# Kernel tuning notes

Hardware: AMD Instinct MI355X
Metric: run time of the kernel (lower is better)

The kernel has to match this reference:

```python
import jax, jax.numpy as jnp
import numpy as np

N, C, H, W = 8, 256, 64, 64
Q_REDUCE, K_REDUCE, V_REDUCE = 8, 8, 1


def setup_inputs() -> dict:
    key = jax.random.key(0)
    ks = jax.random.split(key, 6)
    Cq, Ck, Cv = C // Q_REDUCE, C // K_REDUCE, C // V_REDUCE
    s = 0.02
    x = jax.random.normal(ks[0], (N, C, H, W), dtype=jnp.float32)
    Wq = jax.random.normal(ks[1], (Cq, C), dtype=jnp.float32) * s
    Wk = jax.random.normal(ks[2], (Ck, C), dtype=jnp.float32) * s
    Wv = jax.random.normal(ks[3], (Cv, C), dtype=jnp.float32) * s
    Wo = jax.random.normal(ks[4], (C, Cv), dtype=jnp.float32) * s
    gamma = jax.random.normal(ks[5], (), dtype=jnp.float32)  # trained scalar (init 0.0 in torch)
    return {"x": x, "Wq": Wq, "Wk": Wk, "Wv": Wv, "Wo": Wo, "gamma": gamma}


def reference(x, Wq, Wk, Wv, Wo, gamma):
    n, c, h, w = x.shape
    xf = x.reshape(n, c, h * w)                      # [N, C, HW]
    q = jnp.einsum('qc,ncl->nql', Wq, xf)            # [N, Cq, HW] (1x1 conv)
    k = jnp.einsum('kc,ncl->nkl', Wk, xf)            # [N, Ck, HW]
    v = jnp.einsum('vc,ncl->nvl', Wv, xf)            # [N, Cv, HW]
    e = jnp.einsum('nci,ncj->nij', q, k)             # [N, HW, HW], unscaled energies
    a = jax.nn.softmax(e, axis=-1)                   # softmax over keys j
    o = jnp.einsum('nvi,nij->nvj', v, a)             # [N, Cv, HW]  (o = bmm(v, a))
    o = o.reshape(n, -1, w, h)                       # faithful: view(N,-1,W,H)
    out = jnp.einsum('ov,nvhw->nohw', Wo, o)         # output 1x1 conv
    return gamma * out
```

## Files before the change

kernel.cpp:

```cpp
#include <hip/hip_runtime.h>
#include <hip/hip_bf16.h>

#define NB 8
#define CIN 256
#define LL 4096
#define CQ 32
#define CV 256

typedef __attribute__((ext_vector_type(8))) short bf16x8;
typedef __attribute__((ext_vector_type(4))) float f32x4;

__device__ __forceinline__ unsigned short f2bf(float f) {
    union { __hip_bfloat16 h; unsigned short u; } c;
    c.h = __float2bfloat16(f);
    return c.u;
}
__device__ __forceinline__ float bf2f(unsigned short h) {
    return __uint_as_float(((unsigned)h) << 16);
}

__global__ __launch_bounds__(256) void k_wcast(
    const float* __restrict__ Wq, const float* __restrict__ Wk,
    const float* __restrict__ Wv, const float* __restrict__ Wo,
    unsigned short* __restrict__ Wb, unsigned short* __restrict__ Wob)
{
    const float LOG2E = 1.4426950408889634f;
    const int row = blockIdx.x, t = threadIdx.x;
    if (row < 320) {
        float val;
        if (row < 32)      val = Wq[row * 256 + t] * LOG2E;
        else if (row < 64) val = Wk[(row - 32) * 256 + t];
        else               val = Wv[(row - 64) * 256 + t];
        Wb[row * 256 + t] = f2bf(val);
    } else {
        const int r2 = row - 320;
        Wob[r2 * 256 + t] = f2bf(Wo[r2 * 256 + t]);
    }
}

__global__ __launch_bounds__(512) void k_qkv3(
    const float* __restrict__ x, const unsigned short* __restrict__ Wb,
    unsigned short* __restrict__ qkt, unsigned short* __restrict__ v)
{
    __shared__ unsigned short xlds[64][264];
    __shared__ unsigned short tr[64][72];
    const int n = blockIdx.y, l0 = blockIdx.x * 64, t = threadIdx.x;
    const int w = t >> 6, lane = t & 63, lid = lane & 15, quad = lane >> 4;

    #pragma unroll
    for (int part = 0; part < 4; part++) {
        const int cbase = part * 64 + w * 8;
        float tmp[8];
        #pragma unroll
        for (int cc = 0; cc < 8; cc++)
            tmp[cc] = x[((size_t)n * CIN + cbase + cc) * LL + l0 + lane];
        bf16x8 s;
        #pragma unroll
        for (int cc = 0; cc < 8; cc++) s[cc] = (short)f2bf(tmp[cc]);
        *(bf16x8*)&xlds[lane][cbase] = s;
    }
    __syncthreads();

    const f32x4 fzero = {0.f, 0.f, 0.f, 0.f};
    f32x4 acc[3][4];
    #pragma unroll
    for (int mt = 0; mt < 3; mt++)
        #pragma unroll
        for (int nt = 0; nt < 4; nt++) acc[mt][nt] = fzero;

    for (int k0 = 0; k0 < 256; k0 += 32) {
        bf16x8 bx[4];
        #pragma unroll
        for (int nt = 0; nt < 4; nt++)
            bx[nt] = *(const bf16x8*)&xlds[nt * 16 + lid][k0 + quad * 8];
        #pragma unroll
        for (int vt = 0; vt < 2; vt++) {
            const bf16x8 wa = *(const bf16x8*)&Wb[(64 + w * 32 + vt * 16 + lid) * 256 + k0 + quad * 8];
            #pragma unroll
            for (int nt = 0; nt < 4; nt++)
                acc[vt][nt] = __builtin_amdgcn_mfma_f32_16x16x32_bf16(wa, bx[nt], acc[vt][nt], 0, 0, 0);
        }
        if (w < 4) {
            const bf16x8 wa = *(const bf16x8*)&Wb[(w * 16 + lid) * 256 + k0 + quad * 8];
            #pragma unroll
            for (int nt = 0; nt < 4; nt++)
                acc[2][nt] = __builtin_amdgcn_mfma_f32_16x16x32_bf16(wa, bx[nt], acc[2][nt], 0, 0, 0);
        }
    }
    #pragma unroll
    for (int vt = 0; vt < 2; vt++)
        #pragma unroll
        for (int nt = 0; nt < 4; nt++)
            #pragma unroll
            for (int reg = 0; reg < 4; reg++) {
                const int vr = w * 32 + vt * 16 + quad * 4 + reg;
                v[((size_t)n * CV + vr) * LL + l0 + nt * 16 + lid] = f2bf(acc[vt][nt][reg]);
            }
    if (w < 4) {
        #pragma unroll
        for (int nt = 0; nt < 4; nt++)
            #pragma unroll
            for (int reg = 0; reg < 4; reg++)
                tr[nt * 16 + lid][w * 16 + quad * 4 + reg] = f2bf(acc[2][nt][reg]);
    }
    __syncthreads();
    {
        const int l = t >> 3, c = (t & 7) * 8;
        *(uint4*)&qkt[((size_t)n * LL + l0 + l) * 64 + c] = *(const uint4*)&tr[l][c];
    }
}

__global__ __launch_bounds__(512) void k_rowsum3(
    const unsigned short* __restrict__ qkt, float* __restrict__ lns)
{
    __shared__ float red[64];
    const int n = blockIdx.y, i0 = blockIdx.x * 64, t = threadIdx.x;
    const int w = t >> 6, lid = t & 15, quad = (t & 63) >> 4;
    if (t < 64) red[t] = 0.f;
    __syncthreads();

    bf16x8 aq[4];
    #pragma unroll
    for (int mt = 0; mt < 4; mt++)
        aq[mt] = *(const bf16x8*)&qkt[((size_t)n * LL + i0 + mt * 16 + lid) * 64 + quad * 8];

    const f32x4 fzero = {0.f, 0.f, 0.f, 0.f};
    float sums[4][4];
    #pragma unroll
    for (int mt = 0; mt < 4; mt++)
        #pragma unroll
        for (int reg = 0; reg < 4; reg++) sums[mt][reg] = 0.f;

    for (int jt = 0; jt < 8; jt++) {
        const int j0 = jt * 512 + w * 64;
        bf16x8 bk[4];
        #pragma unroll
        for (int nt = 0; nt < 4; nt++)
            bk[nt] = *(const bf16x8*)&qkt[((size_t)n * LL + j0 + nt * 16 + lid) * 64 + 32 + quad * 8];
        #pragma unroll
        for (int mt = 0; mt < 4; mt++)
            #pragma unroll
            for (int nt = 0; nt < 4; nt++) {
                f32x4 e = __builtin_amdgcn_mfma_f32_16x16x32_bf16(aq[mt], bk[nt], fzero, 0, 0, 0);
                sums[mt][0] += __builtin_amdgcn_exp2f(e[0]);
                sums[mt][1] += __builtin_amdgcn_exp2f(e[1]);
                sums[mt][2] += __builtin_amdgcn_exp2f(e[2]);
                sums[mt][3] += __builtin_amdgcn_exp2f(e[3]);
            }
    }
    #pragma unroll
    for (int mt = 0; mt < 4; mt++)
        #pragma unroll
        for (int reg = 0; reg < 4; reg++) {
            float s = sums[mt][reg];
            s += __shfl_xor(s, 1); s += __shfl_xor(s, 2);
            s += __shfl_xor(s, 4); s += __shfl_xor(s, 8);
            if (lid == 0) atomicAdd(&red[mt * 16 + quad * 4 + reg], s);
        }
    __syncthreads();
    if (t < 64) lns[(size_t)n * LL + i0 + t] = -__builtin_log2f(red[t]);
}

__global__ __launch_bounds__(512, 4) void k_attn8(
    const unsigned short* __restrict__ qkt, const unsigned short* __restrict__ v,
    const float* __restrict__ lns, const unsigned short* __restrict__ Wob,
    const float* __restrict__ gp, float* __restrict__ out)
{
    __shared__ unsigned short pbuf[2][4][4][64][8];
    __shared__ unsigned short olds[64][264];

    const int bid = blockIdx.x;
    const int n = bid & 7, j0 = (bid >> 3) * 64, t = threadIdx.x;
    const int w = t >> 6, lane = t & 63, lid = lane & 15, quad = lane >> 4;
    const int kbw = w >> 1;
    const int qr = (w & 1) * 2 + (quad >> 1);
    const int e0 = (quad & 1) * 4;

    const unsigned short* qrow = qkt + ((size_t)n * LL + w * 16 + lid) * 64 + quad * 8;
    const float* lrow = lns + (size_t)n * LL + w * 16 + quad * 4;
    const unsigned short* vrow = v + ((size_t)n * CV + w * 32 + lid) * LL + quad * 8;

    bf16x8 bk[4];
    #pragma unroll
    for (int nt = 0; nt < 4; nt++)
        bk[nt] = *(const bf16x8*)&qkt[((size_t)n * LL + j0 + nt * 16 + lid) * 64 + 32 + quad * 8];

    const f32x4 fzero = {0.f, 0.f, 0.f, 0.f};
    f32x4 acc[2][4];
    #pragma unroll
    for (int mt = 0; mt < 2; mt++)
        #pragma unroll
        for (int nt = 0; nt < 4; nt++) acc[mt][nt] = fzero;

    bf16x8 aq = *(const bf16x8*)qrow;
    f32x4 lnsC = *(const f32x4*)lrow;
    {
        f32x4 e[4];
        #pragma unroll
        for (int nt = 0; nt < 4; nt++)
            e[nt] = __builtin_amdgcn_mfma_f32_16x16x32_bf16(aq, bk[nt], lnsC, 0, 0, 0);
        aq = *(const bf16x8*)(qrow + (size_t)128 * 64);
        lnsC = *(const f32x4*)(lrow + 128);
        #pragma unroll
        for (int nt = 0; nt < 4; nt++) {
            ushort4 s;
            s.x = f2bf(__builtin_amdgcn_exp2f(e[nt][0]));
            s.y = f2bf(__builtin_amdgcn_exp2f(e[nt][1]));
            s.z = f2bf(__builtin_amdgcn_exp2f(e[nt][2]));
            s.w = f2bf(__builtin_amdgcn_exp2f(e[nt][3]));
            *(ushort4*)&pbuf[0][nt][kbw][qr * 16 + lid][e0] = s;
        }
    }
    bf16x8 av[8];
    #pragma unroll
    for (int mt = 0; mt < 2; mt++)
        #pragma unroll
        for (int h = 0; h < 4; h++)
            av[mt * 4 + h] = *(const bf16x8*)(vrow + (size_t)mt * 16 * LL + h * 32);
    __syncthreads();

    for (int ic = 0; ic < 31; ic++) {
        const int cur = ic & 1;
        const size_t i0 = (size_t)ic * 128;
        f32x4 e2[4];
        #pragma unroll
        for (int nt = 0; nt < 4; nt++)
            e2[nt] = __builtin_amdgcn_mfma_f32_16x16x32_bf16(aq, bk[nt], lnsC, 0, 0, 0);
        const size_t ipf = (ic < 30) ? (i0 + 256) : i0;
        aq = *(const bf16x8*)(qrow + ipf * 64);
        lnsC = *(const f32x4*)(lrow + ipf);
        #pragma unroll
        for (int nt = 0; nt < 4; nt++) {
            ushort4 s;
            s.x = f2bf(__builtin_amdgcn_exp2f(e2[nt][0]));
            s.y = f2bf(__builtin_amdgcn_exp2f(e2[nt][1]));
            s.z = f2bf(__builtin_amdgcn_exp2f(e2[nt][2]));
            s.w = f2bf(__builtin_amdgcn_exp2f(e2[nt][3]));
            *(ushort4*)&pbuf[cur ^ 1][nt][kbw][qr * 16 + lid][e0] = s;
        }
        #pragma unroll
        for (int h = 0; h < 4; h++) {
            bf16x8 bp[4];
            #pragma unroll
            for (int nt = 0; nt < 4; nt++)
                bp[nt] = *(const bf16x8*)&pbuf[cur][nt][h][lane][0];
            #pragma unroll
            for (int mt = 0; mt < 2; mt++)
                #pragma unroll
                for (int nt = 0; nt < 4; nt++)
                    acc[mt][nt] = __builtin_amdgcn_mfma_f32_16x16x32_bf16(av[mt * 4 + h], bp[nt], acc[mt][nt], 0, 0, 0);
            #pragma unroll
            for (int mt = 0; mt < 2; mt++)
                av[mt * 4 + h] = *(const bf16x8*)(vrow + (size_t)mt * 16 * LL + (i0 + 128) + h * 32);
        }
        __syncthreads();
    }
    #pragma unroll
    for (int h = 0; h < 4; h++) {
        bf16x8 bp[4];
        #pragma unroll
        for (int nt = 0; nt < 4; nt++)
            bp[nt] = *(const bf16x8*)&pbuf[1][nt][h][lane][0];
        #pragma unroll
        for (int mt = 0; mt < 2; mt++)
            #pragma unroll
            for (int nt = 0; nt < 4; nt++)
                acc[mt][nt] = __builtin_amdgcn_mfma_f32_16x16x32_bf16(av[mt * 4 + h], bp[nt], acc[mt][nt], 0, 0, 0);
    }
    __syncthreads();

    #pragma unroll
    for (int mt = 0; mt < 2; mt++)
        #pragma unroll
        for (int nt = 0; nt < 4; nt++) {
            ushort4 s;
            s.x = f2bf(acc[mt][nt][0]); s.y = f2bf(acc[mt][nt][1]);
            s.z = f2bf(acc[mt][nt][2]); s.w = f2bf(acc[mt][nt][3]);
            *(ushort4*)&olds[nt * 16 + lid][w * 32 + mt * 16 + quad * 4] = s;
        }
    __syncthreads();
    f32x4 oacc[2][4];
    #pragma unroll
    for (int mt = 0; mt < 2; mt++)
        #pragma unroll
        for (int nt = 0; nt < 4; nt++) oacc[mt][nt] = fzero;
    for (int k0 = 0; k0 < 256; k0 += 32) {
        bf16x8 bo[4];
        #pragma unroll
        for (int nt = 0; nt < 4; nt++)
            bo[nt] = *(const bf16x8*)&olds[nt * 16 + lid][k0 + quad * 8];
        #pragma unroll
        for (int mt = 0; mt < 2; mt++) {
            const bf16x8 wa = *(const bf16x8*)&Wob[(w * 32 + mt * 16 + lid) * 256 + k0 + quad * 8];
            #pragma unroll
            for (int nt = 0; nt < 4; nt++)
                oacc[mt][nt] = __builtin_amdgcn_mfma_f32_16x16x32_bf16(wa, bo[nt], oacc[mt][nt], 0, 0, 0);
        }
    }
    const float g = *gp;
    #pragma unroll
    for (int mt = 0; mt < 2; mt++)
        #pragma unroll
        for (int nt = 0; nt < 4; nt++)
            #pragma unroll
            for (int reg = 0; reg < 4; reg++) {
                const int r = w * 32 + mt * 16 + quad * 4 + reg;
                out[((size_t)n * CIN + r) * LL + j0 + nt * 16 + lid] = g * oacc[mt][nt][reg];
            }
}

extern "C" void kernel_launch(void* const* d_in, const int* in_sizes, int n_in,
                              void* d_out, int out_size, void* d_ws, size_t ws_size,
                              hipStream_t stream) {
    const float* x     = (const float*)d_in[0];
    const float* Wq    = (const float*)d_in[1];
    const float* Wk    = (const float*)d_in[2];
    const float* Wv    = (const float*)d_in[3];
    const float* Wo    = (const float*)d_in[4];
    const float* gamma = (const float*)d_in[5];

    unsigned short* qkt = (unsigned short*)d_ws;
    unsigned short* v   = qkt + (size_t)NB * LL * 64;
    unsigned short* Wb  = v + (size_t)NB * CV * LL;
    unsigned short* Wob = Wb + 320 * 256;
    float* lns          = (float*)(Wob + 256 * 256);
    float* out = (float*)d_out;

    k_wcast  <<<dim3(576),   256, 0, stream>>>(Wq, Wk, Wv, Wo, Wb, Wob);
    k_qkv3   <<<dim3(64, 8), 512, 0, stream>>>(x, Wb, qkt, v);
    k_rowsum3<<<dim3(64, 8), 512, 0, stream>>>(qkt, lns);
    k_attn8  <<<dim3(512),   512, 0, stream>>>(qkt, v, lns, Wob, gamma, out);
}
```

Baseline: 263.4 us.

## Halve attention output tile to 32 columns, double grid, shrink V register prefetch

```diff
diff --git a/kernel.cpp b/kernel.cpp
--- a/kernel.cpp
+++ b/kernel.cpp
@@ -161,16 +161,16 @@
     if (t < 64) lns[(size_t)n * LL + i0 + t] = -__builtin_log2f(red[t]);
 }
 
-__global__ __launch_bounds__(512, 4) void k_attn8(
+__global__ __launch_bounds__(512, 6) void k_attn11(
     const unsigned short* __restrict__ qkt, const unsigned short* __restrict__ v,
     const float* __restrict__ lns, const unsigned short* __restrict__ Wob,
     const float* __restrict__ gp, float* __restrict__ out)
 {
-    __shared__ unsigned short pbuf[2][4][4][64][8];
-    __shared__ unsigned short olds[64][264];
+    __shared__ unsigned short pbuf[2][2][4][64][8];
+    __shared__ unsigned short olds[32][264];
 
     const int bid = blockIdx.x;
-    const int n = bid & 7, j0 = (bid >> 3) * 64, t = threadIdx.x;
+    const int n = bid & 7, j0 = (bid >> 3) * 32, t = threadIdx.x;
     const int w = t >> 6, lane = t & 63, lid = lane & 15, quad = lane >> 4;
     const int kbw = w >> 1;
     const int qr = (w & 1) * 2 + (quad >> 1);
@@ -180,29 +180,33 @@
     const float* lrow = lns + (size_t)n * LL + w * 16 + quad * 4;
     const unsigned short* vrow = v + ((size_t)n * CV + w * 32 + lid) * LL + quad * 8;
 
-    bf16x8 bk[4];
-    #pragma unroll
-    for (int nt = 0; nt < 4; nt++)
+    bf16x8 bk[2];
+    #pragma unroll
+    for (int nt = 0; nt < 2; nt++)
         bk[nt] = *(const bf16x8*)&qkt[((size_t)n * LL + j0 + nt * 16 + lid) * 64 + 32 + quad * 8];
 
     const f32x4 fzero = {0.f, 0.f, 0.f, 0.f};
-    f32x4 acc[2][4];
-    #pragma unroll
-    for (int mt = 0; mt < 2; mt++)
-        #pragma unroll
-        for (int nt = 0; nt < 4; nt++) acc[mt][nt] = fzero;
+    f32x4 acc[2][2];
+    #pragma unroll
+    for (int mt = 0; mt < 2; mt++)
+        #pragma unroll
+        for (int nt = 0; nt < 2; nt++) acc[mt][nt] = fzero;
 
     bf16x8 aq = *(const bf16x8*)qrow;
     f32x4 lnsC = *(const f32x4*)lrow;
+    bf16x8 avA[2], avB[2];
+    #pragma unroll
+    for (int mt = 0; mt < 2; mt++)
+        avA[mt] = *(const bf16x8*)(vrow + (size_t)mt * 16 * LL + 0);
     {
-        f32x4 e[4];
-        #pragma unroll
-        for (int nt = 0; nt < 4; nt++)
+        f32x4 e[2];
+        #pragma unroll
+        for (int nt = 0; nt < 2; nt++)
             e[nt] = __builtin_amdgcn_mfma_f32_16x16x32_bf16(aq, bk[nt], lnsC, 0, 0, 0);
         aq = *(const bf16x8*)(qrow + (size_t)128 * 64);
         lnsC = *(const f32x4*)(lrow + 128);
         #pragma unroll
-        for (int nt = 0; nt < 4; nt++) {
+        for (int nt = 0; nt < 2; nt++) {
             ushort4 s;
             s.x = f2bf(__builtin_amdgcn_exp2f(e[nt][0]));
             s.y = f2bf(__builtin_amdgcn_exp2f(e[nt][1]));
@@ -211,26 +215,20 @@
             *(ushort4*)&pbuf[0][nt][kbw][qr * 16 + lid][e0] = s;
         }
     }
-    bf16x8 av[8];
-    #pragma unroll
-    for (int mt = 0; mt < 2; mt++)
-        #pragma unroll
-        for (int h = 0; h < 4; h++)
-            av[mt * 4 + h] = *(const bf16x8*)(vrow + (size_t)mt * 16 * LL + h * 32);
     __syncthreads();
 
     for (int ic = 0; ic < 31; ic++) {
         const int cur = ic & 1;
         const size_t i0 = (size_t)ic * 128;
-        f32x4 e2[4];
-        #pragma unroll
-        for (int nt = 0; nt < 4; nt++)
+        f32x4 e2[2];
+        #pragma unroll
+        for (int nt = 0; nt < 2; nt++)
             e2[nt] = __builtin_amdgcn_mfma_f32_16x16x32_bf16(aq, bk[nt], lnsC, 0, 0, 0);
         const size_t ipf = (ic < 30) ? (i0 + 256) : i0;
         aq = *(const bf16x8*)(qrow + ipf * 64);
         lnsC = *(const f32x4*)(lrow + ipf);
         #pragma unroll
-        for (int nt = 0; nt < 4; nt++) {
+        for (int nt = 0; nt < 2; nt++) {
             ushort4 s;
             s.x = f2bf(__builtin_amdgcn_exp2f(e2[nt][0]));
             s.y = f2bf(__builtin_amdgcn_exp2f(e2[nt][1]));
@@ -238,62 +236,125 @@
             s.w = f2bf(__builtin_amdgcn_exp2f(e2[nt][3]));
             *(ushort4*)&pbuf[cur ^ 1][nt][kbw][qr * 16 + lid][e0] = s;
         }
-        #pragma unroll
-        for (int h = 0; h < 4; h++) {
-            bf16x8 bp[4];
-            #pragma unroll
-            for (int nt = 0; nt < 4; nt++)
-                bp[nt] = *(const bf16x8*)&pbuf[cur][nt][h][lane][0];
-            #pragma unroll
-            for (int mt = 0; mt < 2; mt++)
-                #pragma unroll
-                for (int nt = 0; nt < 4; nt++)
-                    acc[mt][nt] = __builtin_amdgcn_mfma_f32_16x16x32_bf16(av[mt * 4 + h], bp[nt], acc[mt][nt], 0, 0, 0);
-            #pragma unroll
-            for (int mt = 0; mt < 2; mt++)
-                av[mt * 4 + h] = *(const bf16x8*)(vrow + (size_t)mt * 16 * LL + (i0 + 128) + h * 32);
-        }
+        bf16x8 bp[2];
+        #pragma unroll
+        for (int mt = 0; mt < 2; mt++)
+            avB[mt] = *(const bf16x8*)(vrow + (size_t)mt * 16 * LL + i0 + 32);
+        #pragma unroll
+        for (int nt = 0; nt < 2; nt++)
+            bp[nt] = *(const bf16x8*)&pbuf[cur][nt][0][lane][0];
+        #pragma unroll
+        for (int mt = 0; mt < 2; mt++)
+            #pragma unroll
+            for (int nt = 0; nt < 2; nt++)
+                acc[mt][nt] = __builtin_amdgcn_mfma_f32_16x16x32_bf16(avA[mt], bp[nt], acc[mt][nt], 0, 0, 0);
+        #pragma unroll
+        for (int mt = 0; mt < 2; mt++)
+            avA[mt] = *(const bf16x8*)(vrow + (size_t)mt * 16 * LL + i0 + 64);
+        #pragma unroll
+        for (int nt = 0; nt < 2; nt++)
+            bp[nt] = *(const bf16x8*)&pbuf[cur][nt][1][lane][0];
+        #pragma unroll
+        for (int mt = 0; mt < 2; mt++)
+            #pragma unroll
+            for (int nt = 0; nt < 2; nt++)
+                acc[mt][nt] = __builtin_amdgcn_mfma_f32_16x16x32_bf16(avB[mt], bp[nt], acc[mt][nt], 0, 0, 0);
+        #pragma unroll
+        for (int mt = 0; mt < 2; mt++)
+            avB[mt] = *(const bf16x8*)(vrow + (size_t)mt * 16 * LL + i0 + 96);
+        #pragma unroll
+        for (int nt = 0; nt < 2; nt++)
+            bp[nt] = *(const bf16x8*)&pbuf[cur][nt][2][lane][0];
+        #pragma unroll
+        for (int mt = 0; mt < 2; mt++)
+            #pragma unroll
+            for (int nt = 0; nt < 2; nt++)
+                acc[mt][nt] = __builtin_amdgcn_mfma_f32_16x16x32_bf16(avA[mt], bp[nt], acc[mt][nt], 0, 0, 0);
+        #pragma unroll
+        for (int mt = 0; mt < 2; mt++)
+            avA[mt] = *(const bf16x8*)(vrow + (size_t)mt * 16 * LL + i0 + 128);
+        #pragma unroll
+        for (int nt = 0; nt < 2; nt++)
+            bp[nt] = *(const bf16x8*)&pbuf[cur][nt][3][lane][0];
+        #pragma unroll
+        for (int mt = 0; mt < 2; mt++)
+            #pragma unroll
+            for (int nt = 0; nt < 2; nt++)
+                acc[mt][nt] = __builtin_amdgcn_mfma_f32_16x16x32_bf16(avB[mt], bp[nt], acc[mt][nt], 0, 0, 0);
         __syncthreads();
     }
-    #pragma unroll
-    for (int h = 0; h < 4; h++) {
-        bf16x8 bp[4];
-        #pragma unroll
-        for (int nt = 0; nt < 4; nt++)
-            bp[nt] = *(const bf16x8*)&pbuf[1][nt][h][lane][0];
-        #pragma unroll
-        for (int mt = 0; mt < 2; mt++)
-            #pragma unroll
-            for (int nt = 0; nt < 4; nt++)
-                acc[mt][nt] = __builtin_amdgcn_mfma_f32_16x16x32_bf16(av[mt * 4 + h], bp[nt], acc[mt][nt], 0, 0, 0);
-    }
-    __syncthreads();
-
-    #pragma unroll
-    for (int mt = 0; mt < 2; mt++)
-        #pragma unroll
-        for (int nt = 0; nt < 4; nt++) {
+    {
+        const size_t i0 = (size_t)31 * 128;
+        bf16x8 bp[2];
+        #pragma unroll
+        for (int mt = 0; mt < 2; mt++)
+            avB[mt] = *(const bf16x8*)(vrow + (size_t)mt * 16 * LL + i0 + 32);
+        #pragma unroll
+        for (int nt = 0; nt < 2; nt++)
+            bp[nt] = *(const bf16x8*)&pbuf[1][nt][0][lane][0];
+        #pragma unroll
+        for (int mt = 0; mt < 2; mt++)
+            #pragma unroll
+            for (int nt = 0; nt < 2; nt++)
+                acc[mt][nt] = __builtin_amdgcn_mfma_f32_16x16x32_bf16(avA[mt], bp[nt], acc[mt][nt], 0, 0, 0);
+        #pragma unroll
+        for (int mt = 0; mt < 2; mt++)
+            avA[mt] = *(const bf16x8*)(vrow + (size_t)mt * 16 * LL + i0 + 64);
+        #pragma unroll
+        for (int nt = 0; nt < 2; nt++)
+            bp[nt] = *(const bf16x8*)&pbuf[1][nt][1][lane][0];
+        #pragma unroll
+        for (int mt = 0; mt < 2; mt++)
+            #pragma unroll
+            for (int nt = 0; nt < 2; nt++)
+                acc[mt][nt] = __builtin_amdgcn_mfma_f32_16x16x32_bf16(avB[mt], bp[nt], acc[mt][nt], 0, 0, 0);
+        #pragma unroll
+        for (int mt = 0; mt < 2; mt++)
+            avB[mt] = *(const bf16x8*)(vrow + (size_t)mt * 16 * LL + i0 + 96);
+        #pragma unroll
+        for (int nt = 0; nt < 2; nt++)
+            bp[nt] = *(const bf16x8*)&pbuf[1][nt][2][lane][0];
+        #pragma unroll
+        for (int mt = 0; mt < 2; mt++)
+            #pragma unroll
+            for (int nt = 0; nt < 2; nt++)
+                acc[mt][nt] = __builtin_amdgcn_mfma_f32_16x16x32_bf16(avA[mt], bp[nt], acc[mt][nt], 0, 0, 0);
+        #pragma unroll
+        for (int nt = 0; nt < 2; nt++)
+            bp[nt] = *(const bf16x8*)&pbuf[1][nt][3][lane][0];
+        #pragma unroll
+        for (int mt = 0; mt < 2; mt++)
+            #pragma unroll
+            for (int nt = 0; nt < 2; nt++)
+                acc[mt][nt] = __builtin_amdgcn_mfma_f32_16x16x32_bf16(avB[mt], bp[nt], acc[mt][nt], 0, 0, 0);
+    }
+    __syncthreads();
+
+    #pragma unroll
+    for (int mt = 0; mt < 2; mt++)
+        #pragma unroll
+        for (int nt = 0; nt < 2; nt++) {
             ushort4 s;
             s.x = f2bf(acc[mt][nt][0]); s.y = f2bf(acc[mt][nt][1]);
             s.z = f2bf(acc[mt][nt][2]); s.w = f2bf(acc[mt][nt][3]);
             *(ushort4*)&olds[nt * 16 + lid][w * 32 + mt * 16 + quad * 4] = s;
         }
     __syncthreads();
-    f32x4 oacc[2][4];
-    #pragma unroll
-    for (int mt = 0; mt < 2; mt++)
-        #pragma unroll
-        for (int nt = 0; nt < 4; nt++) oacc[mt][nt] = fzero;
+    f32x4 oacc[2][2];
+    #pragma unroll
+    for (int mt = 0; mt < 2; mt++)
+        #pragma unroll
+        for (int nt = 0; nt < 2; nt++) oacc[mt][nt] = fzero;
     for (int k0 = 0; k0 < 256; k0 += 32) {
-        bf16x8 bo[4];
-        #pragma unroll
-        for (int nt = 0; nt < 4; nt++)
+        bf16x8 bo[2];
+        #pragma unroll
+        for (int nt = 0; nt < 2; nt++)
             bo[nt] = *(const bf16x8*)&olds[nt * 16 + lid][k0 + quad * 8];
         #pragma unroll
         for (int mt = 0; mt < 2; mt++) {
             const bf16x8 wa = *(const bf16x8*)&Wob[(w * 32 + mt * 16 + lid) * 256 + k0 + quad * 8];
             #pragma unroll
-            for (int nt = 0; nt < 4; nt++)
+            for (int nt = 0; nt < 2; nt++)
                 oacc[mt][nt] = __builtin_amdgcn_mfma_f32_16x16x32_bf16(wa, bo[nt], oacc[mt][nt], 0, 0, 0);
         }
     }
@@ -301,7 +362,7 @@
     #pragma unroll
     for (int mt = 0; mt < 2; mt++)
         #pragma unroll
-        for (int nt = 0; nt < 4; nt++)
+        for (int nt = 0; nt < 2; nt++)
             #pragma unroll
             for (int reg = 0; reg < 4; reg++) {
                 const int r = w * 32 + mt * 16 + quad * 4 + reg;
@@ -329,5 +390,5 @@
     k_wcast  <<<dim3(576),   256, 0, stream>>>(Wq, Wk, Wv, Wo, Wb, Wob);
     k_qkv3   <<<dim3(64, 8), 512, 0, stream>>>(x, Wb, qkt, v);
     k_rowsum3<<<dim3(64, 8), 512, 0, stream>>>(qkt, lns);
-    k_attn8  <<<dim3(512),   512, 0, stream>>>(qkt, v, lns, Wob, gamma, out);
-}
+    k_attn11 <<<dim3(1024),  512, 0, stream>>>(qkt, v, lns, Wob, gamma, out);
+}
```

Result: slower. 399.6 us (+51.7%).

## Rewrite attention kernel with 32x32 MFMA and register-resident probability tiles

Applied to the files above, without the earlier changes.

```diff
diff --git a/kernel.cpp b/kernel.cpp
--- a/kernel.cpp
+++ b/kernel.cpp
@@ -9,14 +9,21 @@
 
 typedef __attribute__((ext_vector_type(8))) short bf16x8;
 typedef __attribute__((ext_vector_type(4))) float f32x4;
+typedef __attribute__((ext_vector_type(16))) float f32x16;
 
 __device__ __forceinline__ unsigned short f2bf(float f) {
     union { __hip_bfloat16 h; unsigned short u; } c;
     c.h = __float2bfloat16(f);
     return c.u;
 }
-__device__ __forceinline__ float bf2f(unsigned short h) {
-    return __uint_as_float(((unsigned)h) << 16);
+
+__device__ __forceinline__ unsigned cvtpk(float a, float b) {
+    unsigned r;
+    asm("v_cvt_pk_bf16_f32 %0, %1, %2" : "=v"(r) : "v"(a), "v"(b));
+    return r;
+}
+__device__ __forceinline__ void pl32swap(unsigned &x, unsigned &y) {
+    asm volatile("v_permlane32_swap_b32 %0, %1" : "+v"(x), "+v"(y));
 }
 
 __global__ __launch_bounds__(256) void k_wcast(
@@ -161,152 +168,110 @@
     if (t < 64) lns[(size_t)n * LL + i0 + t] = -__builtin_log2f(red[t]);
 }
 
-__global__ __launch_bounds__(512, 4) void k_attn8(
+__global__ __launch_bounds__(512, 2) void k_attn15(
     const unsigned short* __restrict__ qkt, const unsigned short* __restrict__ v,
     const float* __restrict__ lns, const unsigned short* __restrict__ Wob,
     const float* __restrict__ gp, float* __restrict__ out)
 {
-    __shared__ unsigned short pbuf[2][4][4][64][8];
-    __shared__ unsigned short olds[64][264];
+    __shared__ unsigned short olds[128][264];
 
     const int bid = blockIdx.x;
-    const int n = bid & 7, j0 = (bid >> 3) * 64, t = threadIdx.x;
-    const int w = t >> 6, lane = t & 63, lid = lane & 15, quad = lane >> 4;
-    const int kbw = w >> 1;
-    const int qr = (w & 1) * 2 + (quad >> 1);
-    const int e0 = (quad & 1) * 4;
-
-    const unsigned short* qrow = qkt + ((size_t)n * LL + w * 16 + lid) * 64 + quad * 8;
-    const float* lrow = lns + (size_t)n * LL + w * 16 + quad * 4;
-    const unsigned short* vrow = v + ((size_t)n * CV + w * 32 + lid) * LL + quad * 8;
-
-    bf16x8 bk[4];
-    #pragma unroll
-    for (int nt = 0; nt < 4; nt++)
-        bk[nt] = *(const bf16x8*)&qkt[((size_t)n * LL + j0 + nt * 16 + lid) * 64 + 32 + quad * 8];
-
-    const f32x4 fzero = {0.f, 0.f, 0.f, 0.f};
-    f32x4 acc[2][4];
-    #pragma unroll
-    for (int mt = 0; mt < 2; mt++)
-        #pragma unroll
-        for (int nt = 0; nt < 4; nt++) acc[mt][nt] = fzero;
-
-    bf16x8 aq = *(const bf16x8*)qrow;
-    f32x4 lnsC = *(const f32x4*)lrow;
-    {
-        f32x4 e[4];
-        #pragma unroll
-        for (int nt = 0; nt < 4; nt++)
-            e[nt] = __builtin_amdgcn_mfma_f32_16x16x32_bf16(aq, bk[nt], lnsC, 0, 0, 0);
-        aq = *(const bf16x8*)(qrow + (size_t)128 * 64);
-        lnsC = *(const f32x4*)(lrow + 128);
-        #pragma unroll
-        for (int nt = 0; nt < 4; nt++) {
-            ushort4 s;
-            s.x = f2bf(__builtin_amdgcn_exp2f(e[nt][0]));
-            s.y = f2bf(__builtin_amdgcn_exp2f(e[nt][1]));
-            s.z = f2bf(__builtin_amdgcn_exp2f(e[nt][2]));
-            s.w = f2bf(__builtin_amdgcn_exp2f(e[nt][3]));
-            *(ushort4*)&pbuf[0][nt][kbw][qr * 16 + lid][e0] = s;
-        }
-    }
-    bf16x8 av[8];
-    #pragma unroll
-    for (int mt = 0; mt < 2; mt++)
-        #pragma unroll
-        for (int h = 0; h < 4; h++)
-            av[mt * 4 + h] = *(const bf16x8*)(vrow + (size_t)mt * 16 * LL + h * 32);
-    __syncthreads();
-
-    for (int ic = 0; ic < 31; ic++) {
-        const int cur = ic & 1;
-        const size_t i0 = (size_t)ic * 128;
-        f32x4 e2[4];
-        #pragma unroll
-        for (int nt = 0; nt < 4; nt++)
-            e2[nt] = __builtin_amdgcn_mfma_f32_16x16x32_bf16(aq, bk[nt], lnsC, 0, 0, 0);
-        const size_t ipf = (ic < 30) ? (i0 + 256) : i0;
-        aq = *(const bf16x8*)(qrow + ipf * 64);
-        lnsC = *(const f32x4*)(lrow + ipf);
-        #pragma unroll
-        for (int nt = 0; nt < 4; nt++) {
-            ushort4 s;
-            s.x = f2bf(__builtin_amdgcn_exp2f(e2[nt][0]));
-            s.y = f2bf(__builtin_amdgcn_exp2f(e2[nt][1]));
-            s.z = f2bf(__builtin_amdgcn_exp2f(e2[nt][2]));
-            s.w = f2bf(__builtin_amdgcn_exp2f(e2[nt][3]));
-            *(ushort4*)&pbuf[cur ^ 1][nt][kbw][qr * 16 + lid][e0] = s;
-        }
-        #pragma unroll
-        for (int h = 0; h < 4; h++) {
-            bf16x8 bp[4];
-            #pragma unroll
-            for (int nt = 0; nt < 4; nt++)
-                bp[nt] = *(const bf16x8*)&pbuf[cur][nt][h][lane][0];
-            #pragma unroll
-            for (int mt = 0; mt < 2; mt++)
-                #pragma unroll
-                for (int nt = 0; nt < 4; nt++)
-                    acc[mt][nt] = __builtin_amdgcn_mfma_f32_16x16x32_bf16(av[mt * 4 + h], bp[nt], acc[mt][nt], 0, 0, 0);
-            #pragma unroll
-            for (int mt = 0; mt < 2; mt++)
-                av[mt * 4 + h] = *(const bf16x8*)(vrow + (size_t)mt * 16 * LL + (i0 + 128) + h * 32);
-        }
-        __syncthreads();
-    }
-    #pragma unroll
-    for (int h = 0; h < 4; h++) {
-        bf16x8 bp[4];
-        #pragma unroll
-        for (int nt = 0; nt < 4; nt++)
-            bp[nt] = *(const bf16x8*)&pbuf[1][nt][h][lane][0];
-        #pragma unroll
-        for (int mt = 0; mt < 2; mt++)
-            #pragma unroll
-            for (int nt = 0; nt < 4; nt++)
-                acc[mt][nt] = __builtin_amdgcn_mfma_f32_16x16x32_bf16(av[mt * 4 + h], bp[nt], acc[mt][nt], 0, 0, 0);
-    }
-    __syncthreads();
-
-    #pragma unroll
-    for (int mt = 0; mt < 2; mt++)
-        #pragma unroll
-        for (int nt = 0; nt < 4; nt++) {
-            ushort4 s;
-            s.x = f2bf(acc[mt][nt][0]); s.y = f2bf(acc[mt][nt][1]);
-            s.z = f2bf(acc[mt][nt][2]); s.w = f2bf(acc[mt][nt][3]);
-            *(ushort4*)&olds[nt * 16 + lid][w * 32 + mt * 16 + quad * 4] = s;
-        }
-    __syncthreads();
-    f32x4 oacc[2][4];
-    #pragma unroll
-    for (int mt = 0; mt < 2; mt++)
-        #pragma unroll
-        for (int nt = 0; nt < 4; nt++) oacc[mt][nt] = fzero;
-    for (int k0 = 0; k0 < 256; k0 += 32) {
-        bf16x8 bo[4];
-        #pragma unroll
-        for (int nt = 0; nt < 4; nt++)
-            bo[nt] = *(const bf16x8*)&olds[nt * 16 + lid][k0 + quad * 8];
-        #pragma unroll
-        for (int mt = 0; mt < 2; mt++) {
-            const bf16x8 wa = *(const bf16x8*)&Wob[(w * 32 + mt * 16 + lid) * 256 + k0 + quad * 8];
-            #pragma unroll
-            for (int nt = 0; nt < 4; nt++)
-                oacc[mt][nt] = __builtin_amdgcn_mfma_f32_16x16x32_bf16(wa, bo[nt], oacc[mt][nt], 0, 0, 0);
-        }
-    }
+    const int n = bid & 7, jblk = bid >> 3;
+    const int t = threadIdx.x;
+    const int w = t >> 6, lane = t & 63, l31 = lane & 31, hi = lane >> 5;
+    const int jt = w >> 1, vh = w & 1;
+    const int j0w = jblk * 128 + jt * 32;
+    const int v0w = vh * 128;
+
+    const bf16x8 bk0 = *(const bf16x8*)&qkt[((size_t)n * LL + j0w + l31) * 64 + 32 + hi * 8];
+    const bf16x8 bk1 = *(const bf16x8*)&qkt[((size_t)n * LL + j0w + l31) * 64 + 48 + hi * 8];
+
+    const unsigned short* qbase = qkt + (size_t)n * LL * 64;
+    const float* lbase = lns + (size_t)n * LL;
+    const unsigned short* vbase = v + ((size_t)n * CV + v0w + l31) * LL;
+
+    f32x16 oacc0, oacc1, oacc2, oacc3;
+    #pragma unroll
+    for (int r = 0; r < 16; r++) { oacc0[r] = 0.f; oacc1[r] = 0.f; oacc2[r] = 0.f; oacc3[r] = 0.f; }
+
+    for (int ic = 0; ic < 128; ic++) {
+        const int i0 = ic * 32;
+        const bf16x8 aq0 = *(const bf16x8*)&qbase[((size_t)(i0 + l31)) * 64 + hi * 8];
+        const bf16x8 aq1 = *(const bf16x8*)&qbase[((size_t)(i0 + l31)) * 64 + 16 + hi * 8];
+        f32x16 e;
+        {
+            const f32x4 g0 = *(const f32x4*)&lbase[i0 + 0 + hi * 4];
+            const f32x4 g1 = *(const f32x4*)&lbase[i0 + 8 + hi * 4];
+            const f32x4 g2 = *(const f32x4*)&lbase[i0 + 16 + hi * 4];
+            const f32x4 g3 = *(const f32x4*)&lbase[i0 + 24 + hi * 4];
+            e[0] = g0[0];  e[1] = g0[1];  e[2] = g0[2];  e[3] = g0[3];
+            e[4] = g1[0];  e[5] = g1[1];  e[6] = g1[2];  e[7] = g1[3];
+            e[8] = g2[0];  e[9] = g2[1];  e[10] = g2[2]; e[11] = g2[3];
+            e[12] = g3[0]; e[13] = g3[1]; e[14] = g3[2]; e[15] = g3[3];
+        }
+        const bf16x8 bv00 = *(const bf16x8*)(vbase + (size_t)0 * 32 * LL + i0 + hi * 8);
+        const bf16x8 bv01 = *(const bf16x8*)(vbase + (size_t)0 * 32 * LL + i0 + 16 + hi * 8);
+        const bf16x8 bv10 = *(const bf16x8*)(vbase + (size_t)1 * 32 * LL + i0 + hi * 8);
+        const bf16x8 bv11 = *(const bf16x8*)(vbase + (size_t)1 * 32 * LL + i0 + 16 + hi * 8);
+        const bf16x8 bv20 = *(const bf16x8*)(vbase + (size_t)2 * 32 * LL + i0 + hi * 8);
+        const bf16x8 bv21 = *(const bf16x8*)(vbase + (size_t)2 * 32 * LL + i0 + 16 + hi * 8);
+        const bf16x8 bv30 = *(const bf16x8*)(vbase + (size_t)3 * 32 * LL + i0 + hi * 8);
+        const bf16x8 bv31 = *(const bf16x8*)(vbase + (size_t)3 * 32 * LL + i0 + 16 + hi * 8);
+        e = __builtin_amdgcn_mfma_f32_32x32x16_bf16(aq0, bk0, e, 0, 0, 0);
+        e = __builtin_amdgcn_mfma_f32_32x32x16_bf16(aq1, bk1, e, 0, 0, 0);
+        unsigned a0 = cvtpk(__builtin_amdgcn_exp2f(e[0]), __builtin_amdgcn_exp2f(e[1]));
+        unsigned b0 = cvtpk(__builtin_amdgcn_exp2f(e[4]), __builtin_amdgcn_exp2f(e[5]));
+        pl32swap(a0, b0);
+        unsigned a1 = cvtpk(__builtin_amdgcn_exp2f(e[2]), __builtin_amdgcn_exp2f(e[3]));
+        unsigned b1 = cvtpk(__builtin_amdgcn_exp2f(e[6]), __builtin_amdgcn_exp2f(e[7]));
+        pl32swap(a1, b1);
+        unsigned a2 = cvtpk(__builtin_amdgcn_exp2f(e[8]), __builtin_amdgcn_exp2f(e[9]));
+        unsigned b2 = cvtpk(__builtin_amdgcn_exp2f(e[12]), __builtin_amdgcn_exp2f(e[13]));
+        pl32swap(a2, b2);
+        unsigned a3 = cvtpk(__builtin_amdgcn_exp2f(e[10]), __builtin_amdgcn_exp2f(e[11]));
+        unsigned b3 = cvtpk(__builtin_amdgcn_exp2f(e[14]), __builtin_amdgcn_exp2f(e[15]));
+        pl32swap(a3, b3);
+        union { unsigned u[4]; bf16x8 v8; } pa0c, pa1c;
+        pa0c.u[0] = a0; pa0c.u[1] = a1; pa0c.u[2] = b0; pa0c.u[3] = b1;
+        pa1c.u[0] = a2; pa1c.u[1] = a3; pa1c.u[2] = b2; pa1c.u[3] = b3;
+        const bf16x8 pa0 = pa0c.v8, pa1 = pa1c.v8;
+        oacc0 = __builtin_amdgcn_mfma_f32_32x32x16_bf16(pa0, bv00, oacc0, 0, 0, 0);
+        oacc0 = __builtin_amdgcn_mfma_f32_32x32x16_bf16(pa1, bv01, oacc0, 0, 0, 0);
+        oacc1 = __builtin_amdgcn_mfma_f32_32x32x16_bf16(pa0, bv10, oacc1, 0, 0, 0);
+        oacc1 = __builtin_amdgcn_mfma_f32_32x32x16_bf16(pa1, bv11, oacc1, 0, 0, 0);
+        oacc2 = __builtin_amdgcn_mfma_f32_32x32x16_bf16(pa0, bv20, oacc2, 0, 0, 0);
+        oacc2 = __builtin_amdgcn_mfma_f32_32x32x16_bf16(pa1, bv21, oacc2, 0, 0, 0);
+        oacc3 = __builtin_amdgcn_mfma_f32_32x32x16_bf16(pa0, bv30, oacc3, 0, 0, 0);
+        oacc3 = __builtin_amdgcn_mfma_f32_32x32x16_bf16(pa1, bv31, oacc3, 0, 0, 0);
+        if ((ic & 3) == 3) __builtin_amdgcn_s_barrier();
+    }
+
+    #pragma unroll
+    for (int r = 0; r < 16; r++) {
+        const int jl = jt * 32 + (r & 3) + 8 * (r >> 2) + 4 * hi;
+        olds[jl][v0w + 0 * 32 + l31] = f2bf(oacc0[r]);
+        olds[jl][v0w + 1 * 32 + l31] = f2bf(oacc1[r]);
+        olds[jl][v0w + 2 * 32 + l31] = f2bf(oacc2[r]);
+        olds[jl][v0w + 3 * 32 + l31] = f2bf(oacc3[r]);
+    }
+    __syncthreads();
     const float g = *gp;
-    #pragma unroll
-    for (int mt = 0; mt < 2; mt++)
-        #pragma unroll
-        for (int nt = 0; nt < 4; nt++)
-            #pragma unroll
-            for (int reg = 0; reg < 4; reg++) {
-                const int r = w * 32 + mt * 16 + quad * 4 + reg;
-                out[((size_t)n * CIN + r) * LL + j0 + nt * 16 + lid] = g * oacc[mt][nt][reg];
-            }
+    for (int jt2 = 0; jt2 < 4; jt2++) {
+        f32x16 oc;
+        #pragma unroll
+        for (int r = 0; r < 16; r++) oc[r] = 0.f;
+        #pragma unroll
+        for (int kk = 0; kk < 16; kk++) {
+            const bf16x8 wa = *(const bf16x8*)&Wob[(w * 32 + l31) * 256 + kk * 16 + hi * 8];
+            const bf16x8 ob = *(const bf16x8*)&olds[jt2 * 32 + l31][kk * 16 + hi * 8];
+            oc = __builtin_amdgcn_mfma_f32_32x32x16_bf16(wa, ob, oc, 0, 0, 0);
+        }
+        #pragma unroll
+        for (int r = 0; r < 16; r++) {
+            const int rr = w * 32 + (r & 3) + 8 * (r >> 2) + 4 * hi;
+            out[((size_t)n * CIN + rr) * LL + jblk * 128 + jt2 * 32 + l31] = g * oc[r];
+        }
+    }
 }
 
 extern "C" void kernel_launch(void* const* d_in, const int* in_sizes, int n_in,
@@ -329,5 +294,5 @@
     k_wcast  <<<dim3(576),   256, 0, stream>>>(Wq, Wk, Wv, Wo, Wb, Wob);
     k_qkv3   <<<dim3(64, 8), 512, 0, stream>>>(x, Wb, qkt, v);
     k_rowsum3<<<dim3(64, 8), 512, 0, stream>>>(qkt, lns);
-    k_attn8  <<<dim3(512),   512, 0, stream>>>(qkt, v, lns, Wob, gamma, out);
-}
+    k_attn15 <<<dim3(256),   512, 0, stream>>>(qkt, v, lns, Wob, gamma, out);
+}
```

New measurement: 451.4 us. 71.4% more time.
